# Kernel optimization log

Hardware: AMD Instinct MI355X
Metric: run time of the kernel (lower is better)

Reference implementation:

```python
import jax, jax.numpy as jnp
import numpy as np

# Dims: N batch, I input channels, C = in/hidden/attention/projection/out channels (all 128),
# streams=1, groups=1, spatial kernel 3, dropout 0.
N, I, C, H, W = 8, 128, 128, 36, 36


def _conv(x, w, pad):
    # x: [N, Cin, H, W], w: [Cout, Cin, kh, kw]
    return jax.lax.conv_general_dilated(
        x, w, (1, 1), pad, dimension_numbers=("NCHW", "OIHW", "NCHW"))


def _bias(b):
    return b[None, :, None, None]


def setup_inputs() -> dict:
    key = jax.random.key(0)
    ks = jax.random.split(key, 16)
    std = 0.05

    def w(k, o, i, s):
        return jax.random.normal(k, (o, i, s, s), jnp.float32) * std

    p = {}
    p["inp"] = jax.random.normal(ks[0], (N, I, H, W), jnp.float32)
    p["c0"] = jax.random.normal(ks[1], (1, C, 1, 1), jnp.float32)
    # proj_x: 1x1 conv input->in_channels, bias init 0
    p["w_x"] = w(ks[2], C, I, 1)
    p["b_x"] = jnp.zeros((C,), jnp.float32)
    # token convs (3x3, no bias); q uses SAME pad, k/v VALID
    p["w_qx"] = w(ks[3], C, C, 3)
    p["w_qc"] = w(ks[4], C, C, 3)
    scale = C ** (-0.5)  # gain = attn_channels^-0.5 on k projections
    p["w_kx"] = w(ks[5], C, C, 3) * scale
    p["w_kc"] = w(ks[6], C, C, 3) * scale
    p["w_vx"] = w(ks[7], C, C, 3)
    p["w_vc"] = w(ks[8], C, C, 3)
    # gating 1x1 convs: proj_z (bias=init_gate=1), proj_n (bias=0), in 2*proj channels
    p["w_z"] = w(ks[9], C, 2 * C, 1)
    p["b_z"] = jnp.ones((C,), jnp.float32)
    p["w_n"] = w(ks[10], C, 2 * C, 1)
    p["b_n"] = jnp.zeros((C,), jnp.float32)
    # proj_h: in_channels + 2*projection_channels -> hidden
    p["w_h"] = w(ks[11], C, 3 * C, 1)
    p["b_h"] = jnp.zeros((C,), jnp.float32)
    # output 1x1 conv hidden -> out_channels
    p["w_o"] = w(ks[12], C, C, 1)
    p["b_o"] = jnp.zeros((C,), jnp.float32)
    return p


def reference(inp, c0, w_x, b_x, w_qx, w_qc, w_kx, w_kc, w_vx, w_vc,
              w_z, b_z, w_n, b_n, w_h, b_h, w_o, b_o):
    # proj_x (1x1) -> x: [N, C, H, W]
    x = _conv(inp, w_x, "VALID") + _bias(b_x)
    n_, _, hh, ww = x.shape
    c = jnp.broadcast_to(c0, (n_, c0.shape[1], hh, ww))
    q_len = hh * ww
    # q: SAME pad -> Q = H*W tokens; k/v: VALID -> D = (H-2)*(W-2) tokens
    q = jnp.stack([_conv(x, w_qx, "SAME"), _conv(c, w_qc, "SAME")], 0)
    q = q.reshape(2, n_, -1, q_len)                      # [A, N, C, Q]
    k_x = _conv(x, w_kx, "VALID")
    d_len = k_x.shape[2] * k_x.shape[3]
    k = jnp.stack([k_x, _conv(c, w_kc, "VALID")], 0).reshape(2, n_, -1, d_len)   # [B, N, C, D]
    v = jnp.stack([_conv(x, w_vx, "VALID"), _conv(c, w_vc, "VALID")], 0)
    v = v.reshape(2, n_, -1, d_len)                      # [B, N, C, D]
    # all (A query source) x (B key/value source) attention pairs
    attn = jax.nn.softmax(jnp.einsum("ancq,bncd->anbqd", q, k), axis=-1)
    a = jnp.einsum("bncd,anbqd->anbcq", v, attn)         # [A, N, B, C, Q]
    a = a.reshape(2, n_, -1, hh, ww)                     # channels = B*C = 2*proj
    a_x, a_c = a[0], a[1]
    # GRU-style gated cell update (stored state; not part of the returned output)
    z = jax.nn.sigmoid(_conv(a_c, w_z, "VALID") + _bias(b_z))
    n_cand = jnp.tanh(_conv(a_c, w_n, "VALID") + _bias(b_n))
    c_new = z * c + (1.0 - z) * n_cand  # noqa: F841 (past['c'] in the original)
    # hidden: tanh(proj_h(cat[x, a_x])), dropout p=0 is identity
    xa = jnp.concatenate([x, a_x], axis=1)               # [N, 3*C, H, W]
    h = jnp.tanh(_conv(xa, w_h, "VALID") + _bias(b_h))
    return _conv(h, w_o, "VALID") + _bias(b_o)           # [N, C, H, W]
```

## Files before the change

### kernel.cpp

```cpp
#include <hip/hip_runtime.h>
#include <hip/hip_bf16.h>
#include <math.h>

#define NN 8
#define CH 128
#define HH 36
#define WWI 36
#define PP 1296
#define DD 1156
#define VP 1280
#define KC 1152
#define QT 81
#define DT 5

typedef __attribute__((ext_vector_type(8))) short short8;
typedef __attribute__((ext_vector_type(4))) float f32x4;
typedef __attribute__((ext_vector_type(8))) _Float16 half8;

__device__ inline unsigned short f2bf(float f) {
    __hip_bfloat16 h = __float2bfloat16(f);
    return __builtin_bit_cast(unsigned short, h);
}
__device__ inline float fast_tanh(float x) {
    float e = __expf(2.f * x);
    return 1.f - 2.f / (e + 1.f);
}
#define MFMA(a, b, c) __builtin_amdgcn_mfma_f32_16x16x32_bf16((a), (b), (c), 0, 0, 0)

__global__ __launch_bounds__(256)
void k_setup(const float* __restrict__ wq, const float* __restrict__ wk,
             const float* __restrict__ wv, const float* __restrict__ wh,
             const float* __restrict__ wo, const float* __restrict__ wx,
             const float* __restrict__ c0, const float* __restrict__ w_vc,
             const float* __restrict__ b_h,
             unsigned short* __restrict__ wcat, unsigned short* __restrict__ whb,
             unsigned short* __restrict__ wob,
             float* __restrict__ hconst,
             const float* __restrict__ inp, const float* __restrict__ bx,
             unsigned short* __restrict__ xt)
{
    if (blockIdx.x >= 577) {
        const int t = threadIdx.x;
        const int wave = t >> 6, lane = t & 63;
        const int pid = (blockIdx.x - 577) * 4 + wave;
        const int n = pid / 162;
        const int rem = pid - n * 162;
        const int by = rem / 81;
        const int qg = rem - by * 81;
        const int quad = lane >> 4, lrow = lane & 15;
        const int p0 = qg * 16;
        const int co0 = by * 64;
        const float* in_n = inp + (size_t)n * CH * PP;
        f32x4 acc[4] = {};

#pragma unroll
        for (int ks = 0; ks < 4; ++ks) {
            union { short8 v; unsigned short u[8]; } a;
            int ci0 = ks * 32 + quad * 8;
#pragma unroll
            for (int j = 0; j < 8; ++j)
                a.u[j] = f2bf(in_n[(size_t)(ci0 + j) * PP + p0 + lrow]);
#pragma unroll
            for (int ni = 0; ni < 4; ++ni) {
                const float* wrow = wx + (size_t)(co0 + ni * 16 + lrow) * CH + ks * 32 + quad * 8;
                float4 f0 = *(const float4*)wrow;
                float4 f1 = *(const float4*)(wrow + 4);
                union { short8 v; unsigned short u[8]; } b;
                b.u[0] = f2bf(f0.x); b.u[1] = f2bf(f0.y);
                b.u[2] = f2bf(f0.z); b.u[3] = f2bf(f0.w);
                b.u[4] = f2bf(f1.x); b.u[5] = f2bf(f1.y);
                b.u[6] = f2bf(f1.z); b.u[7] = f2bf(f1.w);
                acc[ni] = MFMA(a.v, b.v, acc[ni]);
            }
        }
        unsigned short* xn = xt + (size_t)n * PP * CH;
#pragma unroll
        for (int ni = 0; ni < 4; ++ni) {
            float bv = bx[co0 + ni * 16 + lrow];
#pragma unroll
            for (int r = 0; r < 4; ++r)
                xn[(size_t)(p0 + quad * 4 + r) * CH + co0 + ni * 16 + lrow] = f2bf(acc[ni][r] + bv);
        }
        return;
    }
    if (blockIdx.x == 576) {
        __shared__ float c0s[CH];
        __shared__ float part[256];
        __shared__ float vcs[CH];
        const int t = threadIdx.x;
        const int c = t & 127, half = t >> 7;
        if (t < CH) c0s[t] = c0[t];
        __syncthreads();
        {
            const float* row = w_vc + (size_t)c * 1152 + half * 576;
            float s = 0.f;
#pragma unroll 4
            for (int j4 = 0; j4 < 144; ++j4) {
                float4 v = ((const float4*)row)[j4];
                int j = half * 576 + j4 * 4;
                s += v.x * c0s[j / 9] + v.y * c0s[(j + 1) / 9]
                   + v.z * c0s[(j + 2) / 9] + v.w * c0s[(j + 3) / 9];
            }
            part[t] = s;
        }
        __syncthreads();
        if (t < CH) vcs[t] = part[t] + part[t + 128];
        __syncthreads();
        {
            const float* wrow = wh + (size_t)c * 384 + 256 + half * 64;
            float hs = 0.f;
#pragma unroll
            for (int j4 = 0; j4 < 16; ++j4) {
                float4 v = ((const float4*)wrow)[j4];
                int ci = half * 64 + j4 * 4;
                hs += v.x * vcs[ci] + v.y * vcs[ci + 1] + v.z * vcs[ci + 2] + v.w * vcs[ci + 3];
            }
            part[t] = hs;
        }
        __syncthreads();
        if (t < CH) hconst[t] = b_h[t] + part[t] + part[t + 128];
        return;
    }
    int t = blockIdx.x * 256 + threadIdx.x;
    int co = t / KC;
    int rem = t - co * KC;
    int tap = rem >> 7, ci = rem & 127;
    int iidx = co * KC + ci * 9 + tap;
    wcat[t] = f2bf(wq[iidx]);
    wcat[147456 + t] = f2bf(wk[iidx]);
    wcat[294912 + t] = f2bf(wv[iidx]);
    if (t < 32768) {
        int c2 = t >> 8, k2 = t & 255;
        whb[t] = f2bf(wh[c2 * 384 + k2]);
    }
    if (t < 16384) wob[t] = f2bf(wo[t]);
}

__global__ __launch_bounds__(256)
void k_conv(const unsigned short* __restrict__ xt, const unsigned short* __restrict__ wcat,
            unsigned short* __restrict__ qt, unsigned short* __restrict__ kt,
            unsigned short* __restrict__ vb)
{
    __shared__ unsigned short lA[2][64 * 40];
    __shared__ unsigned short lB[2][128 * 40];
    const int t = threadIdx.x;
    const int wave = t >> 6, lane = t & 63;
    const int quad = lane >> 4, lrow = lane & 15;
    const int mode = blockIdx.y;
    const int n = blockIdx.z;
    const int limit = (mode == 0) ? PP : DD;
    const int tile0 = blockIdx.x * 64;
    if (tile0 >= limit) return;
    const unsigned short* xn = xt + (size_t)n * PP * CH;
    const unsigned short* wb = wcat + (size_t)mode * 128 * KC;

    const int arow = t >> 2, aseg = t & 3;
    int apr, apc;
    {
        int tok = tile0 + arow; if (tok >= limit) tok = limit - 1;
        int dv = (mode == 0) ? 36 : 34;
        apr = tok / dv; apc = tok - apr * dv;
    }

    uint4 ra, rb0, rb1;
    auto loadChunk = [&](int ks) {
        int tap = ks >> 2;
        int ky = tap / 3, kx = tap - ky * 3;
        int ci = (ks & 3) * 32 + aseg * 8;
        if (mode == 0) {
            int yy = apr + ky - 1, xx = apc + kx - 1;
            bool ok = (yy >= 0) && (yy < HH) && (xx >= 0) && (xx < WWI);
            ra = make_uint4(0, 0, 0, 0);
            if (ok) ra = *(const uint4*)&xn[(size_t)(yy * WWI + xx) * CH + ci];
        } else {
            int yy = apr + ky, xx = apc + kx;
            ra = *(const uint4*)&xn[(size_t)(yy * WWI + xx) * CH + ci];
        }
        rb0 = *(const uint4*)&wb[(size_t)arow * KC + ks * 32 + aseg * 8];
        rb1 = *(const uint4*)&wb[(size_t)(arow + 64) * KC + ks * 32 + aseg * 8];
    };
    auto storeChunk = [&](int buf) {
        *(uint4*)&lA[buf][arow * 40 + aseg * 8] = ra;
        *(uint4*)&lB[buf][arow * 40 + aseg * 8] = rb0;
        *(uint4*)&lB[buf][(arow + 64) * 40 + aseg * 8] = rb1;
    };

    f32x4 acc[4][2] = {};
    loadChunk(0);
    storeChunk(0);
    __syncthreads();

#pragma unroll
    for (int ks = 0; ks < 36; ++ks) {
        const int buf = ks & 1;
        if (ks < 35) loadChunk(ks + 1);
        short8 b0 = *(const short8*)&lB[buf][((wave * 2) * 16 + lrow) * 40 + quad * 8];
        short8 b1 = *(const short8*)&lB[buf][((wave * 2 + 1) * 16 + lrow) * 40 + quad * 8];
#pragma unroll
        for (int mi = 0; mi < 4; ++mi) {
            short8 a = *(const short8*)&lA[buf][(mi * 16 + lrow) * 40 + quad * 8];
            acc[mi][0] = MFMA(a, b0, acc[mi][0]);
            acc[mi][1] = MFMA(a, b1, acc[mi][1]);
        }
        if (ks < 35) storeChunk(buf ^ 1);
        __syncthreads();
    }

    if (mode == 0) {
        unsigned short* qn = qt + (size_t)n * PP * CH;
#pragma unroll
        for (int mi = 0; mi < 4; ++mi)
#pragma unroll
            for (int r = 0; r < 4; ++r) {
                int p = tile0 + mi * 16 + quad * 4 + r;
                if (p < PP)
#pragma unroll
                    for (int ni = 0; ni < 2; ++ni)
                        qn[(size_t)p * CH + (wave * 2 + ni) * 16 + lrow] = f2bf(acc[mi][ni][r]);
            }
    } else if (mode == 1) {
        unsigned short* kn = kt + (size_t)n * DD * CH;
#pragma unroll
        for (int mi = 0; mi < 4; ++mi)
#pragma unroll
            for (int r = 0; r < 4; ++r) {
                int d = tile0 + mi * 16 + quad * 4 + r;
                if (d < DD)
#pragma unroll
                    for (int ni = 0; ni < 2; ++ni)
                        kn[(size_t)d * CH + (wave * 2 + ni) * 16 + lrow] = f2bf(acc[mi][ni][r]);
            }
    } else {
        unsigned short* vn = vb + (size_t)n * CH * VP;
#pragma unroll
        for (int mi = 0; mi < 4; ++mi)
#pragma unroll
            for (int r = 0; r < 4; ++r) {
                int d = tile0 + mi * 16 + quad * 4 + r;
                if (d < DD)
#pragma unroll
                    for (int ni = 0; ni < 2; ++ni)
                        vn[(size_t)((wave * 2 + ni) * 16 + lrow) * VP + d] = f2bf(acc[mi][ni][r]);
            }
    }
}

__global__ __launch_bounds__(256)
void k_attn(const unsigned short* __restrict__ qt, const unsigned short* __restrict__ kt,
            const unsigned short* __restrict__ vb, _Float16* __restrict__ po,
            float* __restrict__ pm, float* __restrict__ pl)
{
    __shared__ unsigned short lS[2][128 * 40];
    __shared__ unsigned short lp[4][16 * 136];
    const int t = threadIdx.x;
    const int wave = t >> 6, lane = t & 63;
    const int quad = lane >> 4, lrow = lane & 15;
    const int qg = blockIdx.x;
    const int dt = blockIdx.y;
    const int n = blockIdx.z;
    const int qti = qg * 4 + wave;
    const int d0 = dt * 256;
    const unsigned short* qn = qt + (size_t)n * PP * CH;
    const unsigned short* kn = kt + (size_t)n * DD * CH;
    const unsigned short* vn = vb + (size_t)n * CH * VP;

    const int arow = t >> 2, aseg8 = (t & 3) * 8;
    const int lo0 = arow * 40 + aseg8;
    const int lo1 = (arow + 64) * 40 + aseg8;

    short8 qa[4];
    {
        int qrow = qti * 16 + lrow; if (qrow >= PP) qrow = PP - 1;
#pragma unroll
        for (int ks = 0; ks < 4; ++ks)
            qa[ks] = *(const short8*)&qn[(size_t)qrow * CH + ks * 32 + quad * 8];
    }

    f32x4 o[8] = {};
    float mx[4] = {-1e30f, -1e30f, -1e30f, -1e30f};
    float rs[4] = {0.f, 0.f, 0.f, 0.f};

#pragma unroll
    for (int h = 0; h < 2; ++h) {
        const int dbase = d0 + h * 128;
        int kr0 = dbase + arow;      if (kr0 >= DD) kr0 = DD - 1;
        int kr1 = dbase + arow + 64; if (kr1 >= DD) kr1 = DD - 1;
        const unsigned short* kp0 = kn + (size_t)kr0 * CH + aseg8;
        const unsigned short* kp1 = kn + (size_t)kr1 * CH + aseg8;
        const unsigned short* vp0 = vn + (size_t)arow * VP + dbase + aseg8;
        const unsigned short* vp1 = vn + (size_t)(arow + 64) * VP + dbase + aseg8;

        f32x4 s[8] = {};
        uint4 r0 = *(const uint4*)kp0;
        uint4 r1 = *(const uint4*)kp1;
        *(uint4*)&lS[0][lo0] = r0;
        *(uint4*)&lS[0][lo1] = r1;
        __syncthreads();
#pragma unroll
        for (int ks = 0; ks < 4; ++ks) {
            const int buf = ks & 1;
            if (ks < 3) {
                r0 = *(const uint4*)(kp0 + (ks + 1) * 32);
                r1 = *(const uint4*)(kp1 + (ks + 1) * 32);
            }
#pragma unroll
            for (int ni = 0; ni < 8; ++ni) {
                short8 b = *(const short8*)&lS[buf][(ni * 16 + lrow) * 40 + quad * 8];
                s[ni] = MFMA(qa[ks], b, s[ni]);
            }
            if (ks < 3) {
                *(uint4*)&lS[buf ^ 1][lo0] = r0;
                *(uint4*)&lS[buf ^ 1][lo1] = r1;
            }
            __syncthreads();
        }

#pragma unroll
        for (int ni = 0; ni < 8; ++ni)
            if (dbase + ni * 16 + lrow >= DD)
#pragma unroll
                for (int r = 0; r < 4; ++r) s[ni][r] = -1e30f;

        float hm[4] = {-1e30f, -1e30f, -1e30f, -1e30f};
#pragma unroll
        for (int ni = 0; ni < 8; ++ni)
#pragma unroll
            for (int r = 0; r < 4; ++r) hm[r] = fmaxf(hm[r], s[ni][r]);
#pragma unroll
        for (int off = 1; off < 16; off <<= 1)
#pragma unroll
            for (int r = 0; r < 4; ++r) hm[r] = fmaxf(hm[r], __shfl_xor(hm[r], off, 64));

        float m[4], sc[4];
#pragma unroll
        for (int r = 0; r < 4; ++r) {
            m[r] = fmaxf(mx[r], hm[r]);
            sc[r] = __expf(mx[r] - m[r]);
        }

        float hs[4] = {0.f, 0.f, 0.f, 0.f};
#pragma unroll
        for (int ni = 0; ni < 8; ++ni)
#pragma unroll
            for (int r = 0; r < 4; ++r) {
                float e = __expf(s[ni][r] - m[r]);
                s[ni][r] = e;
                hs[r] += e;
            }
#pragma unroll
        for (int off = 1; off < 16; off <<= 1)
#pragma unroll
            for (int r = 0; r < 4; ++r) hs[r] += __shfl_xor(hs[r], off, 64);
#pragma unroll
        for (int r = 0; r < 4; ++r) {
            rs[r] = rs[r] * sc[r] + hs[r];
            mx[r] = m[r];
        }
#pragma unroll
        for (int ni = 0; ni < 8; ++ni)
#pragma unroll
            for (int r = 0; r < 4; ++r) o[ni][r] *= sc[r];

#pragma unroll
        for (int ni = 0; ni < 8; ++ni)
#pragma unroll
            for (int r = 0; r < 4; ++r)
                lp[wave][(quad * 4 + r) * 136 + ni * 16 + lrow] = f2bf(s[ni][r]);

        r0 = *(const uint4*)vp0;
        r1 = *(const uint4*)vp1;
        *(uint4*)&lS[0][lo0] = r0;
        *(uint4*)&lS[0][lo1] = r1;
        __syncthreads();
#pragma unroll
        for (int ks = 0; ks < 4; ++ks) {
            const int buf = ks & 1;
            if (ks < 3) {
                r0 = *(const uint4*)(vp0 + (ks + 1) * 32);
                r1 = *(const uint4*)(vp1 + (ks + 1) * 32);
            }
            short8 pa = *(const short8*)&lp[wave][lrow * 136 + ks * 32 + quad * 8];
#pragma unroll
            for (int ni = 0; ni < 8; ++ni) {
                short8 b = *(const short8*)&lS[buf][(ni * 16 + lrow) * 40 + quad * 8];
                o[ni] = MFMA(pa, b, o[ni]);
            }
            if (ks < 3) {
                *(uint4*)&lS[buf ^ 1][lo0] = r0;
                *(uint4*)&lS[buf ^ 1][lo1] = r1;
            }
            __syncthreads();
        }
    }

    if (qti < QT) {
        const int base = (n * QT + qti) * DT + dt;
        _Float16* pob = po + (size_t)base * 2048;
#pragma unroll
        for (int ni = 0; ni < 8; ++ni)
#pragma unroll
            for (int r = 0; r < 4; ++r)
                pob[(quad * 4 + r) * 128 + ni * 16 + lrow] = (_Float16)o[ni][r];
        if (lrow == 0)
#pragma unroll
            for (int r = 0; r < 4; ++r) {
                pm[base * 16 + quad * 4 + r] = mx[r];
                pl[base * 16 + quad * 4 + r] = rs[r];
            }
    }
}

__global__ __launch_bounds__(256)
void k_ahout(const _Float16* __restrict__ po, const float* __restrict__ pm,
             const float* __restrict__ pl, const unsigned short* __restrict__ xt,
             const unsigned short* __restrict__ whb, const float* __restrict__ hconst,
             const unsigned short* __restrict__ wob, const float* __restrict__ bo,
             float* __restrict__ out)
{
    __shared__ float sm[80], ssc[80], smg[16], sli[16];
    __shared__ unsigned short la0[16 * 136];
    __shared__ unsigned short lh[16 * 136];
    const int qti = blockIdx.x;
    const int n = blockIdx.y;
    const int base = (n * QT + qti) * DT;
    const int t = threadIdx.x;

    if (t < 80) sm[t] = pm[base * 16 + t];
    __syncthreads();
    if (t < 16) {
        float mg = -1e30f;
#pragma unroll
        for (int dt = 0; dt < DT; ++dt) mg = fmaxf(mg, sm[dt * 16 + t]);
        float ls = 0.f;
#pragma unroll
        for (int dt = 0; dt < DT; ++dt) ls += __expf(sm[dt * 16 + t] - mg) * pl[base * 16 + dt * 16 + t];
        smg[t] = mg; sli[t] = 1.f / ls;
    }
    __syncthreads();
    if (t < 80) ssc[t] = __expf(sm[t] - smg[t & 15]);
    __syncthreads();
    {
        const int row = t >> 4;
        const int c0 = (t & 15) * 8;
        float acc[8] = {};
#pragma unroll
        for (int dt = 0; dt < DT; ++dt) {
            half8 v = *(const half8*)&po[(size_t)(base + dt) * 2048 + t * 8];
            float scv = ssc[dt * 16 + row];
#pragma unroll
            for (int j = 0; j < 8; ++j) acc[j] += scv * (float)v[j];
        }
        float inv = sli[row];
#pragma unroll
        for (int j = 0; j < 8; ++j)
            la0[row * 136 + c0 + j] = f2bf(acc[j] * inv);
    }
    __syncthreads();

    const int wave = t >> 6, lane = t & 63;
    const int quad = lane >> 4, lrow = lane & 15;
    const int p0 = qti * 16;
    const unsigned short* x0 = xt + (size_t)n * PP * CH;

    f32x4 acc1[2] = {};
#pragma unroll
    for (int ks = 0; ks < 8; ++ks) {
        int col = (ks & 3) * 32 + quad * 8;
        short8 a;
        if (ks < 4) a = *(const short8*)&x0[(size_t)(p0 + lrow) * CH + col];
        else        a = *(const short8*)&la0[lrow * 136 + col];
#pragma unroll
        for (int j = 0; j < 2; ++j) {
            int ni = wave * 2 + j;
            short8 b = *(const short8*)&whb[(size_t)(ni * 16 + lrow) * 256 + ks * 32 + quad * 8];
            acc1[j] = MFMA(a, b, acc1[j]);
        }
    }
#pragma unroll
    for (int j = 0; j < 2; ++j) {
        int ni = wave * 2 + j;
        float hc = hconst[ni * 16 + lrow];
#pragma unroll
        for (int r = 0; r < 4; ++r)
            lh[(quad * 4 + r) * 136 + ni * 16 + lrow] = f2bf(fast_tanh(acc1[j][r] + hc));
    }
    __syncthreads();

    f32x4 acc2[2] = {};
#pragma unroll
    for (int ks = 0; ks < 4; ++ks) {
        short8 a = *(const short8*)&lh[lrow * 136 + ks * 32 + quad * 8];
#pragma unroll
        for (int j = 0; j < 2; ++j) {
            int ni = wave * 2 + j;
            short8 b = *(const short8*)&wob[(size_t)(ni * 16 + lrow) * CH + ks * 32 + quad * 8];
            acc2[j] = MFMA(a, b, acc2[j]);
        }
    }
#pragma unroll
    for (int j = 0; j < 2; ++j) {
        int ni = wave * 2 + j;
        float bv = bo[ni * 16 + lrow];
#pragma unroll
        for (int r = 0; r < 4; ++r)
            out[((size_t)(n * CH + ni * 16 + lrow)) * PP + p0 + quad * 4 + r] = acc2[j][r] + bv;
    }
}

extern "C" void kernel_launch(void* const* d_in, const int* in_sizes, int n_in,
                              void* d_out, int out_size, void* d_ws, size_t ws_size,
                              hipStream_t stream)
{
    const float* inp  = (const float*)d_in[0];
    const float* c0   = (const float*)d_in[1];
    const float* w_x  = (const float*)d_in[2];
    const float* b_x  = (const float*)d_in[3];
    const float* w_qx = (const float*)d_in[4];
    const float* w_kx = (const float*)d_in[6];
    const float* w_vx = (const float*)d_in[8];
    const float* w_vc = (const float*)d_in[9];
    const float* w_h  = (const float*)d_in[14];
    const float* b_h  = (const float*)d_in[15];
    const float* w_o  = (const float*)d_in[16];
    const float* b_o  = (const float*)d_in[17];
    float* out = (float*)d_out;

    char* w = (char*)d_ws;
    unsigned short* xt   = (unsigned short*)(w);
    unsigned short* qt   = (unsigned short*)(w + 2654208);
    unsigned short* kt   = (unsigned short*)(w + 5308416);
    unsigned short* vb   = (unsigned short*)(w + 7675904);
    unsigned short* wcat = (unsigned short*)(w + 12951552);
    unsigned short* whb  = (unsigned short*)(w + 13869056);
    unsigned short* wob  = (unsigned short*)(w + 13934592);
    float* hconst        = (float*)(w + 13967360);
    float* pm            = (float*)(w + 13967872);
    float* pl            = (float*)(w + 14382592);
    _Float16* po         = (_Float16*)(w + 14797312);

    hipLaunchKernelGGL(k_setup, dim3(901), dim3(256), 0, stream,
                       w_qx, w_kx, w_vx, w_h, w_o, w_x, c0, w_vc, b_h,
                       wcat, whb, wob, hconst, inp, b_x, xt);

    hipLaunchKernelGGL(k_conv, dim3(21, 3, NN), dim3(256), 0, stream, xt, wcat, qt, kt, vb);

    hipLaunchKernelGGL(k_attn, dim3(21, DT, NN), dim3(256), 0, stream, qt, kt, vb, po, pm, pl);

    hipLaunchKernelGGL(k_ahout, dim3(QT, NN), dim3(256), 0, stream,
                       po, pm, pl, xt, whb, hconst, wob, b_o, out);
}
```

Measured before the change: 186.5 us.

## Fuse split-softmax merge and output projections into attention via last-block counter

Removes the separate k_ahout kernel. Each attention block bumps a per-(batch, query-group) atomic counter, and the last of the DT key-tile blocks to finish merges the partial softmax results. That block then runs the proj_h and output 1x1 GEMMs per wave, using shared memory already allocated for attention. This saves a kernel launch and the inter-kernel gap, at the cost of a serial tail on the last-arriving blocks, more registers (8 accumulators per wave) and reliance on threadfence/atomic ordering.

```diff
diff --git a/kernel.cpp b/kernel.cpp
--- a/kernel.cpp
+++ b/kernel.cpp
@@ -37,7 +37,7 @@
              unsigned short* __restrict__ wob,
              float* __restrict__ hconst,
              const float* __restrict__ inp, const float* __restrict__ bx,
-             unsigned short* __restrict__ xt)
+             unsigned short* __restrict__ xt, int* __restrict__ cnt)
 {
     if (blockIdx.x >= 577) {
         const int t = threadIdx.x;
@@ -121,6 +121,7 @@
         if (t < CH) hconst[t] = b_h[t] + part[t] + part[t + 128];
         return;
     }
+    if (blockIdx.x == 0 && threadIdx.x < 168) cnt[threadIdx.x] = 0;
     int t = blockIdx.x * 256 + threadIdx.x;
     int co = t / KC;
     int rem = t - co * KC;
@@ -248,10 +249,15 @@
 __global__ __launch_bounds__(256)
 void k_attn(const unsigned short* __restrict__ qt, const unsigned short* __restrict__ kt,
             const unsigned short* __restrict__ vb, _Float16* __restrict__ po,
-            float* __restrict__ pm, float* __restrict__ pl)
+            float* __restrict__ pm, float* __restrict__ pl,
+            const unsigned short* __restrict__ xt, const unsigned short* __restrict__ whb,
+            const float* __restrict__ hconst, const unsigned short* __restrict__ wob,
+            const float* __restrict__ bo, float* __restrict__ out,
+            int* __restrict__ cnt)
 {
     __shared__ unsigned short lS[2][128 * 40];
     __shared__ unsigned short lp[4][16 * 136];
+    __shared__ int mflag;
     const int t = threadIdx.x;
     const int wave = t >> 6, lane = t & 63;
     const int quad = lane >> 4, lrow = lane & 15;
@@ -408,102 +414,95 @@
                 pl[base * 16 + quad * 4 + r] = rs[r];
             }
     }
-}
-
-__global__ __launch_bounds__(256)
-void k_ahout(const _Float16* __restrict__ po, const float* __restrict__ pm,
-             const float* __restrict__ pl, const unsigned short* __restrict__ xt,
-             const unsigned short* __restrict__ whb, const float* __restrict__ hconst,
-             const unsigned short* __restrict__ wob, const float* __restrict__ bo,
-             float* __restrict__ out)
-{
-    __shared__ float sm[80], ssc[80], smg[16], sli[16];
-    __shared__ unsigned short la0[16 * 136];
-    __shared__ unsigned short lh[16 * 136];
-    const int qti = blockIdx.x;
-    const int n = blockIdx.y;
-    const int base = (n * QT + qti) * DT;
-    const int t = threadIdx.x;
-
-    if (t < 80) sm[t] = pm[base * 16 + t];
+
+    __threadfence();
+    if (t == 0) mflag = atomicAdd(&cnt[n * 21 + qg], 1);
     __syncthreads();
-    if (t < 16) {
-        float mg = -1e30f;
-#pragma unroll
-        for (int dt = 0; dt < DT; ++dt) mg = fmaxf(mg, sm[dt * 16 + t]);
-        float ls = 0.f;
-#pragma unroll
-        for (int dt = 0; dt < DT; ++dt) ls += __expf(sm[dt * 16 + t] - mg) * pl[base * 16 + dt * 16 + t];
-        smg[t] = mg; sli[t] = 1.f / ls;
-    }
-    __syncthreads();
-    if (t < 80) ssc[t] = __expf(sm[t] - smg[t & 15]);
-    __syncthreads();
-    {
-        const int row = t >> 4;
-        const int c0 = (t & 15) * 8;
-        float acc[8] = {};
-#pragma unroll
-        for (int dt = 0; dt < DT; ++dt) {
-            half8 v = *(const half8*)&po[(size_t)(base + dt) * 2048 + t * 8];
-            float scv = ssc[dt * 16 + row];
-#pragma unroll
-            for (int j = 0; j < 8; ++j) acc[j] += scv * (float)v[j];
-        }
-        float inv = sli[row];
-#pragma unroll
-        for (int j = 0; j < 8; ++j)
-            la0[row * 136 + c0 + j] = f2bf(acc[j] * inv);
-    }
-    __syncthreads();
-
-    const int wave = t >> 6, lane = t & 63;
-    const int quad = lane >> 4, lrow = lane & 15;
+    if (mflag != DT - 1) return;
+    __threadfence();
+    if (qti >= QT) return;
+
+    const int base2 = (n * QT + qti) * DT;
+    const int row = lane >> 2;
+    const int c0 = (lane & 3) * 32;
+
+    float mg = -1e30f;
+#pragma unroll
+    for (int d = 0; d < DT; ++d) mg = fmaxf(mg, pm[base2 * 16 + d * 16 + row]);
+    float ls = 0.f;
+    float sscv[DT];
+#pragma unroll
+    for (int d = 0; d < DT; ++d) {
+        float e = __expf(pm[base2 * 16 + d * 16 + row] - mg);
+        sscv[d] = e;
+        ls += e * pl[base2 * 16 + d * 16 + row];
+    }
+    float inv = 1.f / ls;
+
+    float a0f[32];
+#pragma unroll
+    for (int j = 0; j < 32; ++j) a0f[j] = 0.f;
+#pragma unroll
+    for (int d = 0; d < DT; ++d) {
+        const _Float16* pp = po + (size_t)(base2 + d) * 2048 + row * 128 + c0;
+        float scv = sscv[d];
+#pragma unroll
+        for (int j4 = 0; j4 < 4; ++j4) {
+            half8 v = *(const half8*)(pp + j4 * 8);
+#pragma unroll
+            for (int k = 0; k < 8; ++k) a0f[j4 * 8 + k] += scv * (float)v[k];
+        }
+    }
+#pragma unroll
+    for (int j = 0; j < 32; ++j)
+        lp[wave][row * 136 + c0 + j] = f2bf(a0f[j] * inv);
+    asm volatile("s_waitcnt lgkmcnt(0)" ::: "memory");
+    __builtin_amdgcn_sched_barrier(0);
+
+    const unsigned short* la0w = lp[wave];
+    unsigned short* lhw = &lS[0][0] + wave * 2560;
+    const unsigned short* x0 = xt + (size_t)n * PP * CH;
     const int p0 = qti * 16;
-    const unsigned short* x0 = xt + (size_t)n * PP * CH;
-
-    f32x4 acc1[2] = {};
+
+    f32x4 acc1[8] = {};
 #pragma unroll
     for (int ks = 0; ks < 8; ++ks) {
         int col = (ks & 3) * 32 + quad * 8;
         short8 a;
         if (ks < 4) a = *(const short8*)&x0[(size_t)(p0 + lrow) * CH + col];
-        else        a = *(const short8*)&la0[lrow * 136 + col];
-#pragma unroll
-        for (int j = 0; j < 2; ++j) {
-            int ni = wave * 2 + j;
+        else        a = *(const short8*)&la0w[lrow * 136 + col];
+#pragma unroll
+        for (int ni = 0; ni < 8; ++ni) {
             short8 b = *(const short8*)&whb[(size_t)(ni * 16 + lrow) * 256 + ks * 32 + quad * 8];
-            acc1[j] = MFMA(a, b, acc1[j]);
-        }
-    }
-#pragma unroll
-    for (int j = 0; j < 2; ++j) {
-        int ni = wave * 2 + j;
+            acc1[ni] = MFMA(a, b, acc1[ni]);
+        }
+    }
+#pragma unroll
+    for (int ni = 0; ni < 8; ++ni) {
         float hc = hconst[ni * 16 + lrow];
 #pragma unroll
         for (int r = 0; r < 4; ++r)
-            lh[(quad * 4 + r) * 136 + ni * 16 + lrow] = f2bf(fast_tanh(acc1[j][r] + hc));
-    }
-    __syncthreads();
-
-    f32x4 acc2[2] = {};
+            lhw[(quad * 4 + r) * 136 + ni * 16 + lrow] = f2bf(fast_tanh(acc1[ni][r] + hc));
+    }
+    asm volatile("s_waitcnt lgkmcnt(0)" ::: "memory");
+    __builtin_amdgcn_sched_barrier(0);
+
+    f32x4 acc2[8] = {};
 #pragma unroll
     for (int ks = 0; ks < 4; ++ks) {
-        short8 a = *(const short8*)&lh[lrow * 136 + ks * 32 + quad * 8];
-#pragma unroll
-        for (int j = 0; j < 2; ++j) {
-            int ni = wave * 2 + j;
+        short8 a = *(const short8*)&lhw[lrow * 136 + ks * 32 + quad * 8];
+#pragma unroll
+        for (int ni = 0; ni < 8; ++ni) {
             short8 b = *(const short8*)&wob[(size_t)(ni * 16 + lrow) * CH + ks * 32 + quad * 8];
-            acc2[j] = MFMA(a, b, acc2[j]);
-        }
-    }
-#pragma unroll
-    for (int j = 0; j < 2; ++j) {
-        int ni = wave * 2 + j;
+            acc2[ni] = MFMA(a, b, acc2[ni]);
+        }
+    }
+#pragma unroll
+    for (int ni = 0; ni < 8; ++ni) {
         float bv = bo[ni * 16 + lrow];
 #pragma unroll
         for (int r = 0; r < 4; ++r)
-            out[((size_t)(n * CH + ni * 16 + lrow)) * PP + p0 + quad * 4 + r] = acc2[j][r] + bv;
+            out[((size_t)(n * CH + ni * 16 + lrow)) * PP + p0 + quad * 4 + r] = acc2[ni][r] + bv;
     }
 }
 
@@ -537,15 +536,15 @@
     float* pm            = (float*)(w + 13967872);
     float* pl            = (float*)(w + 14382592);
     _Float16* po         = (_Float16*)(w + 14797312);
+    int* cnt             = (int*)(w + 28068352);
 
     hipLaunchKernelGGL(k_setup, dim3(901), dim3(256), 0, stream,
                        w_qx, w_kx, w_vx, w_h, w_o, w_x, c0, w_vc, b_h,
-                       wcat, whb, wob, hconst, inp, b_x, xt);
+                       wcat, whb, wob, hconst, inp, b_x, xt, cnt);
 
     hipLaunchKernelGGL(k_conv, dim3(21, 3, NN), dim3(256), 0, stream, xt, wcat, qt, kt, vb);
 
-    hipLaunchKernelGGL(k_attn, dim3(21, DT, NN), dim3(256), 0, stream, qt, kt, vb, po, pm, pl);
-
-    hipLaunchKernelGGL(k_ahout, dim3(QT, NN), dim3(256), 0, stream,
-                       po, pm, pl, xt, whb, hconst, wob, b_o, out);
+    hipLaunchKernelGGL(k_attn, dim3(21, DT, NN), dim3(256), 0, stream,
+                       qt, kt, vb, po, pm, pl,
+                       xt, whb, hconst, wob, b_o, out, cnt);
 }
```

Result: slower. 357.4 us (+91.7%).

## Pad x spatially and stream conv tiles via global_load_lds with triple buffering

Applied to the files above, without the earlier changes.

Stores the projected x in a zero-bordered 38x38 layout, so the 3x3 conv no longer needs per-element bounds checks and SAME and VALID modes share one addressing path. The conv kernel now copies A and B tiles straight from global memory into LDS with global_load_lds, using a 3-stage ring buffer and explicit vmcnt waits in place of register staging. The aim is to hide load latency and cut VGPR and instruction overhead in the conv main loop. In exchange, the unpadded LDS rows (stride 32) can cause bank conflicts, the kernel takes extra setup blocks to zero the borders, and correctness depends on the hand-written waitcnt counts.

```diff
diff --git a/kernel.cpp b/kernel.cpp
--- a/kernel.cpp
+++ b/kernel.cpp
@@ -12,6 +12,7 @@
 #define KC 1152
 #define QT 81
 #define DT 5
+#define XPP 1444
 
 typedef __attribute__((ext_vector_type(8))) short short8;
 typedef __attribute__((ext_vector_type(4))) float f32x4;
@@ -26,6 +27,9 @@
     return 1.f - 2.f / (e + 1.f);
 }
 #define MFMA(a, b, c) __builtin_amdgcn_mfma_f32_16x16x32_bf16((a), (b), (c), 0, 0, 0)
+#define GLDS(g, l) __builtin_amdgcn_global_load_lds( \
+    (const __attribute__((address_space(1))) unsigned int*)(g), \
+    (__attribute__((address_space(3))) unsigned int*)(l), 16, 0, 0)
 
 __global__ __launch_bounds__(256)
 void k_setup(const float* __restrict__ wq, const float* __restrict__ wk,
@@ -37,8 +41,22 @@
              unsigned short* __restrict__ wob,
              float* __restrict__ hconst,
              const float* __restrict__ inp, const float* __restrict__ bx,
-             unsigned short* __restrict__ xt)
+             unsigned short* __restrict__ xp)
 {
+    if (blockIdx.x >= 901) {
+        const int n = blockIdx.x - 901;
+        unsigned short* xpn = xp + (size_t)n * XPP * CH;
+        for (int b = threadIdx.x; b < 148 * 16; b += 256) {
+            int cell = b >> 4, part = b & 15;
+            int y, x;
+            if (cell < 38)       { y = 0;              x = cell; }
+            else if (cell < 76)  { y = 37;             x = cell - 38; }
+            else if (cell < 112) { y = cell - 76 + 1;  x = 0; }
+            else                 { y = cell - 112 + 1; x = 37; }
+            *(uint4*)&xpn[((size_t)(y * 38 + x)) * CH + part * 8] = make_uint4(0, 0, 0, 0);
+        }
+        return;
+    }
     if (blockIdx.x >= 577) {
         const int t = threadIdx.x;
         const int wave = t >> 6, lane = t & 63;
@@ -73,13 +91,16 @@
                 acc[ni] = MFMA(a.v, b.v, acc[ni]);
             }
         }
-        unsigned short* xn = xt + (size_t)n * PP * CH;
+        unsigned short* xn = xp + (size_t)n * XPP * CH;
 #pragma unroll
         for (int ni = 0; ni < 4; ++ni) {
             float bv = bx[co0 + ni * 16 + lrow];
 #pragma unroll
-            for (int r = 0; r < 4; ++r)
-                xn[(size_t)(p0 + quad * 4 + r) * CH + co0 + ni * 16 + lrow] = f2bf(acc[ni][r] + bv);
+            for (int r = 0; r < 4; ++r) {
+                int p = p0 + quad * 4 + r;
+                int off = ((p / 36 + 1) * 38 + (p % 36) + 1) * CH;
+                xn[(size_t)off + co0 + ni * 16 + lrow] = f2bf(acc[ni][r] + bv);
+            }
         }
         return;
     }
@@ -137,12 +158,12 @@
 }
 
 __global__ __launch_bounds__(256)
-void k_conv(const unsigned short* __restrict__ xt, const unsigned short* __restrict__ wcat,
+void k_conv(const unsigned short* __restrict__ xp, const unsigned short* __restrict__ wcat,
             unsigned short* __restrict__ qt, unsigned short* __restrict__ kt,
             unsigned short* __restrict__ vb)
 {
-    __shared__ unsigned short lA[2][64 * 40];
-    __shared__ unsigned short lB[2][128 * 40];
+    __shared__ unsigned short lA[3][2048];
+    __shared__ unsigned short lB[3][4096];
     const int t = threadIdx.x;
     const int wave = t >> 6, lane = t & 63;
     const int quad = lane >> 4, lrow = lane & 15;
@@ -151,59 +172,60 @@
     const int limit = (mode == 0) ? PP : DD;
     const int tile0 = blockIdx.x * 64;
     if (tile0 >= limit) return;
-    const unsigned short* xn = xt + (size_t)n * PP * CH;
+    const unsigned short* xn = xp + (size_t)n * XPP * CH;
     const unsigned short* wb = wcat + (size_t)mode * 128 * KC;
 
-    const int arow = t >> 2, aseg = t & 3;
+    const int aseg = t & 3;
     int apr, apc;
     {
-        int tok = tile0 + arow; if (tok >= limit) tok = limit - 1;
+        int tok = tile0 + (t >> 2); if (tok >= limit) tok = limit - 1;
         int dv = (mode == 0) ? 36 : 34;
         apr = tok / dv; apc = tok - apr * dv;
-    }
-
-    uint4 ra, rb0, rb1;
-    auto loadChunk = [&](int ks) {
+        if (mode != 0) { apr += 1; apc += 1; }
+    }
+    const unsigned short* wbr0 = wb + (size_t)(wave * 16 + (lane >> 2)) * KC + (lane & 3) * 8;
+    const unsigned short* wbr1 = wb + (size_t)(64 + wave * 16 + (lane >> 2)) * KC + (lane & 3) * 8;
+    const int ldsA = wave * 512;
+    const int ldsB0 = wave * 512;
+    const int ldsB1 = 2048 + wave * 512;
+
+    auto stage = [&](int ks, int buf) {
         int tap = ks >> 2;
         int ky = tap / 3, kx = tap - ky * 3;
         int ci = (ks & 3) * 32 + aseg * 8;
-        if (mode == 0) {
-            int yy = apr + ky - 1, xx = apc + kx - 1;
-            bool ok = (yy >= 0) && (yy < HH) && (xx >= 0) && (xx < WWI);
-            ra = make_uint4(0, 0, 0, 0);
-            if (ok) ra = *(const uint4*)&xn[(size_t)(yy * WWI + xx) * CH + ci];
-        } else {
-            int yy = apr + ky, xx = apc + kx;
-            ra = *(const uint4*)&xn[(size_t)(yy * WWI + xx) * CH + ci];
-        }
-        rb0 = *(const uint4*)&wb[(size_t)arow * KC + ks * 32 + aseg * 8];
-        rb1 = *(const uint4*)&wb[(size_t)(arow + 64) * KC + ks * 32 + aseg * 8];
+        const unsigned short* srcA = xn + ((size_t)((apr + ky) * 38 + apc + kx)) * CH + ci;
+        int koff = tap * 128 + (ks & 3) * 32;
+        GLDS(srcA, &lA[buf][ldsA]);
+        GLDS(wbr0 + koff, &lB[buf][ldsB0]);
+        GLDS(wbr1 + koff, &lB[buf][ldsB1]);
     };
-    auto storeChunk = [&](int buf) {
-        *(uint4*)&lA[buf][arow * 40 + aseg * 8] = ra;
-        *(uint4*)&lB[buf][arow * 40 + aseg * 8] = rb0;
-        *(uint4*)&lB[buf][(arow + 64) * 40 + aseg * 8] = rb1;
-    };
 
     f32x4 acc[4][2] = {};
-    loadChunk(0);
-    storeChunk(0);
-    __syncthreads();
+    stage(0, 0);
+    stage(1, 1);
+    stage(2, 2);
 
 #pragma unroll
     for (int ks = 0; ks < 36; ++ks) {
-        const int buf = ks & 1;
-        if (ks < 35) loadChunk(ks + 1);
-        short8 b0 = *(const short8*)&lB[buf][((wave * 2) * 16 + lrow) * 40 + quad * 8];
-        short8 b1 = *(const short8*)&lB[buf][((wave * 2 + 1) * 16 + lrow) * 40 + quad * 8];
+        if (ks < 34)      asm volatile("s_waitcnt vmcnt(6)" ::: "memory");
+        else if (ks == 34) asm volatile("s_waitcnt vmcnt(3)" ::: "memory");
+        else               asm volatile("s_waitcnt vmcnt(0)" ::: "memory");
+        __builtin_amdgcn_sched_barrier(0);
+        __builtin_amdgcn_s_barrier();
+        __builtin_amdgcn_sched_barrier(0);
+        const int buf = ks % 3;
+        short8 b0 = *(const short8*)&lB[buf][(wave * 32 + lrow) * 32 + quad * 8];
+        short8 b1 = *(const short8*)&lB[buf][(wave * 32 + 16 + lrow) * 32 + quad * 8];
 #pragma unroll
         for (int mi = 0; mi < 4; ++mi) {
-            short8 a = *(const short8*)&lA[buf][(mi * 16 + lrow) * 40 + quad * 8];
+            short8 a = *(const short8*)&lA[buf][(mi * 16 + lrow) * 32 + quad * 8];
             acc[mi][0] = MFMA(a, b0, acc[mi][0]);
             acc[mi][1] = MFMA(a, b1, acc[mi][1]);
         }
-        if (ks < 35) storeChunk(buf ^ 1);
-        __syncthreads();
+        __builtin_amdgcn_sched_barrier(0);
+        __builtin_amdgcn_s_barrier();
+        __builtin_amdgcn_sched_barrier(0);
+        if (ks < 33) stage(ks + 3, buf);
     }
 
     if (mode == 0) {
@@ -412,7 +434,7 @@
 
 __global__ __launch_bounds__(256)
 void k_ahout(const _Float16* __restrict__ po, const float* __restrict__ pm,
-             const float* __restrict__ pl, const unsigned short* __restrict__ xt,
+             const float* __restrict__ pl, const unsigned short* __restrict__ xp,
              const unsigned short* __restrict__ whb, const float* __restrict__ hconst,
              const unsigned short* __restrict__ wob, const float* __restrict__ bo,
              float* __restrict__ out)
@@ -460,14 +482,16 @@
     const int wave = t >> 6, lane = t & 63;
     const int quad = lane >> 4, lrow = lane & 15;
     const int p0 = qti * 16;
-    const unsigned short* x0 = xt + (size_t)n * PP * CH;
+    const unsigned short* x0 = xp + (size_t)n * XPP * CH;
+    const int ptok = p0 + lrow;
+    const int xoff = ((ptok / 36 + 1) * 38 + (ptok % 36) + 1) * CH;
 
     f32x4 acc1[2] = {};
 #pragma unroll
     for (int ks = 0; ks < 8; ++ks) {
         int col = (ks & 3) * 32 + quad * 8;
         short8 a;
-        if (ks < 4) a = *(const short8*)&x0[(size_t)(p0 + lrow) * CH + col];
+        if (ks < 4) a = *(const short8*)&x0[(size_t)xoff + col];
         else        a = *(const short8*)&la0[lrow * 136 + col];
 #pragma unroll
         for (int j = 0; j < 2; ++j) {
@@ -526,26 +550,26 @@
     float* out = (float*)d_out;
 
     char* w = (char*)d_ws;
-    unsigned short* xt   = (unsigned short*)(w);
-    unsigned short* qt   = (unsigned short*)(w + 2654208);
-    unsigned short* kt   = (unsigned short*)(w + 5308416);
-    unsigned short* vb   = (unsigned short*)(w + 7675904);
-    unsigned short* wcat = (unsigned short*)(w + 12951552);
-    unsigned short* whb  = (unsigned short*)(w + 13869056);
-    unsigned short* wob  = (unsigned short*)(w + 13934592);
-    float* hconst        = (float*)(w + 13967360);
-    float* pm            = (float*)(w + 13967872);
-    float* pl            = (float*)(w + 14382592);
-    _Float16* po         = (_Float16*)(w + 14797312);
-
-    hipLaunchKernelGGL(k_setup, dim3(901), dim3(256), 0, stream,
+    unsigned short* xp   = (unsigned short*)(w);
+    unsigned short* qt   = (unsigned short*)(w + 2957312);
+    unsigned short* kt   = (unsigned short*)(w + 5611520);
+    unsigned short* vb   = (unsigned short*)(w + 7979008);
+    unsigned short* wcat = (unsigned short*)(w + 10600448);
+    unsigned short* whb  = (unsigned short*)(w + 11485184);
+    unsigned short* wob  = (unsigned short*)(w + 11550720);
+    float* hconst        = (float*)(w + 11583488);
+    float* pm            = (float*)(w + 11616256);
+    float* pl            = (float*)(w + 11824128);
+    _Float16* po         = (_Float16*)(w + 12031488);
+
+    hipLaunchKernelGGL(k_setup, dim3(909), dim3(256), 0, stream,
                        w_qx, w_kx, w_vx, w_h, w_o, w_x, c0, w_vc, b_h,
-                       wcat, whb, wob, hconst, inp, b_x, xt);
-
-    hipLaunchKernelGGL(k_conv, dim3(21, 3, NN), dim3(256), 0, stream, xt, wcat, qt, kt, vb);
+                       wcat, whb, wob, hconst, inp, b_x, xp);
+
+    hipLaunchKernelGGL(k_conv, dim3(21, 3, NN), dim3(256), 0, stream, xp, wcat, qt, kt, vb);
 
     hipLaunchKernelGGL(k_attn, dim3(21, DT, NN), dim3(256), 0, stream, qt, kt, vb, po, pm, pl);
 
     hipLaunchKernelGGL(k_ahout, dim3(QT, NN), dim3(256), 0, stream,
-                       po, pm, pl, xt, whb, hconst, wob, b_o, out);
-}
+                       po, pm, pl, xp, whb, hconst, wob, b_o, out);
+}
```

After: 182.8 us (median of 2 runs). 2.0% less time.
